# Kernel optimization log

Measured on AMD Instinct MI355X. Metric: run time of the kernel, lower is better.

## Reference

```python
import jax, jax.numpy as jnp
import numpy as np

SHIFT = 1  # fixed shift_direction (module draws +/-1 at random; we pin +1)

def setup_inputs() -> dict:
    key = jax.random.key(0)
    kx, kw = jax.random.split(key)
    x = jax.random.normal(kx, (1024, 256, 7, 7), dtype=jnp.float32)
    W = jax.random.normal(kw, (128, 3, 3, 512), dtype=jnp.float32)
    return {"x": x, "W": W}

def _fwd(x, W):
    B = x.shape[0]
    t = x.reshape(B, 256, 7, 7)
    # unfold((3,1), padding=(1,0)) along H: t[b,c,k,h,w] = x_pad[b,c,h+k-1,w]
    xp = jnp.pad(t, ((0, 0), (0, 0), (1, 1), (0, 0)))
    t = jnp.stack([xp[:, :, k:k + 7, :] for k in range(3)], axis=2)  # (B,256,3,7,7)
    t = t.reshape(B, 2, 128, 3, 7, 7).transpose(0, 2, 3, 4, 1, 5)   # (B,128,3,7,2,7)
    t = t.reshape(B, 128, 3, 14, 7)
    t = jnp.roll(t, SHIFT, axis=3)
    t = t.reshape(B, 128, 3, 7, 2, 7).sum(axis=4)                   # (B,128,3,7,7)
    t = t.transpose(0, 1, 3, 2, 4)                                  # (B,128,7,3,7)
    t = jnp.roll(t, SHIFT, axis=4)
    # second unfold((3,1), padding=(1,0)) along W dim: gather 3 shifted slices
    tp = jnp.pad(t, ((0, 0), (0, 0), (0, 0), (0, 0), (1, 1)))
    t3 = jnp.stack([tp[..., k2:k2 + 7] for k2 in range(3)], axis=-1)  # (B,128,7,3,7,3) = (m,l,n,j,o,k)
    out = jnp.einsum('mlnjok,ljki->mnoi', t3, W)                     # (B,7,7,512)
    return out.transpose(0, 3, 1, 2)                                 # (B,512,7,7)

def reference(x, W):
    return _fwd(x, W)
```

## Files before the change

kernel.cpp:

```cpp
#include <hip/hip_runtime.h>

typedef __attribute__((ext_vector_type(8)))  __bf16 bvec8;
typedef __attribute__((ext_vector_type(4)))  __bf16 bvec4;
typedef __attribute__((ext_vector_type(16))) float  fvec16;
typedef __attribute__((ext_vector_type(8)))  short  svec8;

__global__ __launch_bounds__(256) void pack_w(const float* __restrict__ W,
                                              __bf16* __restrict__ Wp) {
    int u = blockIdx.x * 256 + threadIdx.x;
    if (u >= 73728) return;
    int lane = u & 63;
    int h    = (u >> 6) & 1;
    int it   = (u >> 7) & 15;
    int t    = u >> 11;
    int i  = (it << 5) + (lane & 31);
    int K0 = ((2 * t + h) << 4) + ((lane >> 5) << 3);
    bvec8 o;
#pragma unroll
    for (int e = 0; e < 8; ++e) {
        int K  = K0 + e;
        int jk = K >> 7;
        int l  = K & 127;
        int j  = (jk * 11) >> 5;
        int k  = jk - 3 * j;
        o[e] = (__bf16)W[((l * 9 + j * 3 + k) << 9) + i];
    }
    *(bvec8*)&Wp[(size_t)u * 8] = o;
}

__global__ __launch_bounds__(512, 4) void conv_mfma(
    const float* __restrict__ x, const __bf16* __restrict__ Wp,
    float* __restrict__ out)
{
    __shared__ __align__(16) char smem[45056];
    __bf16* xs = (__bf16*)smem;
    __bf16* ys = (__bf16*)(smem + 25088);

    const int tid  = threadIdx.x;
    const int lane = tid & 63;
    const int l31  = lane & 31;
    const int ls5  = lane >> 5;
    const int wi   = tid >> 6;
    const int b    = blockIdx.x;

    const float* xb  = x + (size_t)b * 12544;
    const char*  WpB = (const char*)Wp;
    const int wbase  = wi * 4096 + lane * 16;

    bvec8 aE[2][2], aO[2][2];
#pragma unroll
    for (int am = 0; am < 2; ++am)
#pragma unroll
        for (int h = 0; h < 2; ++h) {
            aE[am][h] = *(const bvec8*)(WpB + wbase + am * 2048 + h * 1024);
            aO[am][h] = *(const bvec8*)(WpB + 32768 + wbase + am * 2048 + h * 1024);
        }

    for (int it = 0; it < 7; ++it) {
        int e4 = it * 512 + tid;
        if (e4 < 3136) {
            const float4 v = ((const float4*)xb)[e4];
            bvec4 pk = { (__bf16)v.x, (__bf16)v.y, (__bf16)v.z, (__bf16)v.w };
            *(bvec4*)&xs[e4 * 4] = pk;
        }
    }
    __syncthreads();
    for (int it = 0; it < 3; ++it) {
        int up = it * 512 + tid;
        if (up < 1248) {
            int row  = up >> 4;
            int useg = up & 15;
            int l0   = useg * 8;
            bvec8 ov;
            if (row == 77) {
                ov = __builtin_bit_cast(bvec8, (svec8)0);
            } else if (row < 63) {
                int t = row / 7, w = row - t * 7;
                int tb = t + 5; if (tb >= 7) tb -= 7;
                int cB = tb * 7 + w;
                bool mA = (t >= 1) && (t <= 7);
                int cA = mA ? (t - 1) * 7 + w : 0;
#pragma unroll
                for (int d = 0; d < 8; ++d) {
                    float fa = mA ? (float)xs[(l0 + d) * 49 + cA] : 0.f;
                    float fb = (float)xs[(128 + l0 + d) * 49 + cB];
                    ov[d] = (__bf16)(fa + fb);
                }
            } else if (row < 70) {
                int w = row - 63;
#pragma unroll
                for (int d = 0; d < 8; ++d) ov[d] = xs[(l0 + d) * 49 + w];
            } else {
                int w = row - 70;
#pragma unroll
                for (int d = 0; d < 8; ++d) ov[d] = xs[(l0 + d) * 49 + 7 + w];
            }
            *(bvec8*)&ys[(row << 7) + ((useg ^ (row & 15)) << 3)] = ov;
        }
    }

    int nq[2], oo[2];
#pragma unroll
    for (int sn = 0; sn < 2; ++sn) {
        int s = sn * 32 + l31;
        int sc = (s < 49) ? s : 48;
        nq[sn] = sc / 7;
        oo[sn] = sc - nq[sn] * 7;
    }

    fvec16 acc[2][2];
#pragma unroll
    for (int am = 0; am < 2; ++am)
#pragma unroll
        for (int sn = 0; sn < 2; ++sn)
#pragma unroll
            for (int r = 0; r < 16; ++r) acc[am][sn][r] = 0.f;

    __syncthreads();

    {
        const int zz = (wi & 3) + ((wi >> 2) << 1);
        for (int z = 0; z < zz; ++z) __builtin_amdgcn_s_sleep(8);
    }

#define GEO(JK) {                                                             \
        int j_ = ((JK) * 11) >> 5; int k_ = (JK) - 3 * j_;                    \
        _Pragma("unroll")                                                     \
        for (int sn_ = 0; sn_ < 2; ++sn_) {                                   \
            int tw_ = oo[sn_] + k_ + 5; int w_ = tw_ >= 7 ? tw_ - 7 : tw_;    \
            int row_ = (nq[sn_] + j_) * 7 + w_;                               \
            if (nq[sn_] == 1 && j_ == 0) row_ = 63 + w_;                      \
            if (nq[sn_] == 0 && j_ == 2) row_ = 70 + w_;                      \
            if ((k_ == 0 && oo[sn_] == 0) || (k_ == 2 && oo[sn_] == 6))       \
                row_ = 77;                                                    \
            rowE[sn_] = (row_) << 7; rx[sn_] = row_ & 15; } }

#define STEP(P, AW, TNEXT, DOPF) {                                            \
        _Pragma("unroll")                                                     \
        for (int h_ = 0; h_ < 2; ++h_)                                        \
        _Pragma("unroll")                                                     \
        for (int sn_ = 0; sn_ < 2; ++sn_) {                                   \
            int u_ = ((P) * 4 + h_ * 2 + ls5) ^ rx[sn_];                      \
            bvec8 bf_ = *(const bvec8*)&ys[rowE[sn_] + (u_ << 3)];            \
            __builtin_amdgcn_s_setprio(1);                                    \
            _Pragma("unroll")                                                 \
            for (int am_ = 0; am_ < 2; ++am_)                                 \
                acc[am_][sn_] = __builtin_amdgcn_mfma_f32_32x32x16_bf16(      \
                    AW[am_][h_], bf_, acc[am_][sn_], 0, 0, 0);                \
            __builtin_amdgcn_s_setprio(0);                                    \
        }                                                                     \
        if (DOPF) {                                                           \
            const char* gp_ = WpB + ((size_t)(TNEXT) << 15) + wbase;          \
            _Pragma("unroll")                                                 \
            for (int am_ = 0; am_ < 2; ++am_)                                 \
            _Pragma("unroll")                                                 \
            for (int h_ = 0; h_ < 2; ++h_)                                    \
                AW[am_][h_] = *(const bvec8*)(gp_ + am_ * 2048 + h_ * 1024);  \
        } }

    int rowE[2], rx[2];
    for (int jk = 0; jk < 9; ++jk) {
        const int t0 = jk * 4;
        GEO(jk);
        STEP(0, aE, t0 + 2, true)
        STEP(1, aO, t0 + 3, true)
        STEP(2, aE, t0 + 4, (jk < 8))
        STEP(3, aO, t0 + 5, (jk < 8))
    }

#undef GEO
#undef STEP

    const size_t ob = (size_t)b * 25088;
#pragma unroll
    for (int am = 0; am < 2; ++am) {
        const int i0 = wi * 64 + am * 32 + 4 * ls5;
#pragma unroll
        for (int sn = 0; sn < 2; ++sn) {
            if (sn == 1 && l31 >= 17) continue;
            const int s = sn * 32 + l31;
#pragma unroll
            for (int r = 0; r < 16; ++r) {
                int i = i0 + (r & 3) + 8 * (r >> 2);
                out[ob + (size_t)i * 49 + s] = acc[am][sn][r];
            }
        }
    }
}

extern "C" void kernel_launch(void* const* d_in, const int* in_sizes, int n_in,
                              void* d_out, int out_size, void* d_ws, size_t ws_size,
                              hipStream_t stream) {
    const float* x = (const float*)d_in[0];
    const float* W = (const float*)d_in[1];
    float* out = (float*)d_out;
    __bf16* Wp = (__bf16*)d_ws;
    (void)in_sizes; (void)n_in; (void)out_size; (void)ws_size;

    hipLaunchKernelGGL(pack_w, dim3(288), dim3(256), 0, stream, W, Wp);
    hipLaunchKernelGGL(conv_mfma, dim3(1024), dim3(512), 0, stream, x, Wp, out);
}
```

Before: 96.26 us.

## Tile conv over 4 batches x 256 outputs with LDS-staged double-buffered weights

Each block now handles four batch images and half of the 512 output channels instead of one image and all channels. Weight tiles are streamed into LDS with global_load_lds in a double buffer and shared across all waves, so each weight byte is reused across four images. Before, every wave loaded its own weight fragments from global memory for each image. The cost is large dynamic shared memory (about 142 KB), fewer resident blocks, a barrier after every k-step, and the input-prep phase running serially for the four images.

```diff
diff --git a/kernel.cpp b/kernel.cpp
--- a/kernel.cpp
+++ b/kernel.cpp
@@ -4,17 +4,25 @@
 typedef __attribute__((ext_vector_type(4)))  __bf16 bvec4;
 typedef __attribute__((ext_vector_type(16))) float  fvec16;
 typedef __attribute__((ext_vector_type(8)))  short  svec8;
+
+__device__ __forceinline__ void gload16(const void* g, void* l) {
+    __builtin_amdgcn_global_load_lds(
+        (const __attribute__((address_space(1))) void*)g,
+        (__attribute__((address_space(3))) void*)l,
+        16, 0, 0);
+}
 
 __global__ __launch_bounds__(256) void pack_w(const float* __restrict__ W,
                                               __bf16* __restrict__ Wp) {
     int u = blockIdx.x * 256 + threadIdx.x;
     if (u >= 73728) return;
     int lane = u & 63;
-    int h    = (u >> 6) & 1;
-    int it   = (u >> 7) & 15;
-    int t    = u >> 11;
-    int i  = (it << 5) + (lane & 31);
-    int K0 = ((2 * t + h) << 4) + ((lane >> 5) << 3);
+    int iu   = (u >> 6) & 7;
+    int kk   = (u >> 9) & 3;
+    int ib   = (u >> 11) & 1;
+    int t64  = u >> 12;
+    int i  = ib * 256 + iu * 32 + (lane & 31);
+    int K0 = t64 * 64 + kk * 16 + ((lane >> 5) << 3);
     bvec8 o;
 #pragma unroll
     for (int e = 0; e < 8; ++e) {
@@ -28,75 +36,73 @@
     *(bvec8*)&Wp[(size_t)u * 8] = o;
 }
 
-__global__ __launch_bounds__(512, 4) void conv_mfma(
+__global__ __launch_bounds__(512, 2) void conv_mfma(
     const float* __restrict__ x, const __bf16* __restrict__ Wp,
     float* __restrict__ out)
 {
-    __shared__ __align__(16) char smem[45056];
-    __bf16* xs = (__bf16*)smem;
-    __bf16* ys = (__bf16*)(smem + 25088);
+    extern __shared__ __align__(16) char smem[];
+    __bf16* ys   = (__bf16*)smem;
+    char*  wbufB = smem + 79872;
+    __bf16* xs   = (__bf16*)wbufB;
 
     const int tid  = threadIdx.x;
     const int lane = tid & 63;
     const int l31  = lane & 31;
     const int ls5  = lane >> 5;
-    const int wi   = tid >> 6;
-    const int b    = blockIdx.x;
-
-    const float* xb  = x + (size_t)b * 12544;
+    const int wid  = tid >> 6;
+    const int wq   = wid & 3;
+    const int wm   = wid >> 2;
+    const int bm   = blockIdx.x;
+    const int ib   = blockIdx.y;
+    const int b0   = bm * 4;
+
+    const float* xb  = x + (size_t)b0 * 12544;
     const char*  WpB = (const char*)Wp;
-    const int wbase  = wi * 4096 + lane * 16;
-
-    bvec8 aE[2][2], aO[2][2];
-#pragma unroll
-    for (int am = 0; am < 2; ++am)
-#pragma unroll
-        for (int h = 0; h < 2; ++h) {
-            aE[am][h] = *(const bvec8*)(WpB + wbase + am * 2048 + h * 1024);
-            aO[am][h] = *(const bvec8*)(WpB + 32768 + wbase + am * 2048 + h * 1024);
-        }
-
-    for (int it = 0; it < 7; ++it) {
-        int e4 = it * 512 + tid;
-        if (e4 < 3136) {
-            const float4 v = ((const float4*)xb)[e4];
-            bvec4 pk = { (__bf16)v.x, (__bf16)v.y, (__bf16)v.z, (__bf16)v.w };
-            *(bvec4*)&xs[e4 * 4] = pk;
-        }
-    }
-    __syncthreads();
-    for (int it = 0; it < 3; ++it) {
-        int up = it * 512 + tid;
-        if (up < 1248) {
-            int row  = up >> 4;
-            int useg = up & 15;
-            int l0   = useg * 8;
-            bvec8 ov;
-            if (row == 77) {
-                ov = __builtin_bit_cast(bvec8, (svec8)0);
-            } else if (row < 63) {
-                int t = row / 7, w = row - t * 7;
-                int tb = t + 5; if (tb >= 7) tb -= 7;
-                int cB = tb * 7 + w;
-                bool mA = (t >= 1) && (t <= 7);
-                int cA = mA ? (t - 1) * 7 + w : 0;
-#pragma unroll
-                for (int d = 0; d < 8; ++d) {
-                    float fa = mA ? (float)xs[(l0 + d) * 49 + cA] : 0.f;
-                    float fb = (float)xs[(128 + l0 + d) * 49 + cB];
-                    ov[d] = (__bf16)(fa + fb);
+
+    for (int bb = 0; bb < 4; ++bb) {
+        for (int it = 0; it < 7; ++it) {
+            int e4 = it * 512 + tid;
+            if (e4 < 3136) {
+                const float4 v = ((const float4*)(xb + bb * 12544))[e4];
+                bvec4 pk = { (__bf16)v.x, (__bf16)v.y, (__bf16)v.z, (__bf16)v.w };
+                *(bvec4*)&xs[e4 * 4] = pk;
+            }
+        }
+        __syncthreads();
+        for (int it = 0; it < 3; ++it) {
+            int up = it * 512 + tid;
+            if (up < 1248) {
+                int row  = up >> 4;
+                int useg = up & 15;
+                int l0   = useg * 8;
+                bvec8 ov;
+                if (row == 77) {
+                    ov = __builtin_bit_cast(bvec8, (svec8)0);
+                } else if (row < 63) {
+                    int t = row / 7, w = row - t * 7;
+                    int tb = t + 5; if (tb >= 7) tb -= 7;
+                    int cB = tb * 7 + w;
+                    bool mA = (t >= 1) && (t <= 7);
+                    int cA = mA ? (t - 1) * 7 + w : 0;
+#pragma unroll
+                    for (int d = 0; d < 8; ++d) {
+                        float fa = mA ? (float)xs[(l0 + d) * 49 + cA] : 0.f;
+                        float fb = (float)xs[(128 + l0 + d) * 49 + cB];
+                        ov[d] = (__bf16)(fa + fb);
+                    }
+                } else if (row < 70) {
+                    int w = row - 63;
+#pragma unroll
+                    for (int d = 0; d < 8; ++d) ov[d] = xs[(l0 + d) * 49 + w];
+                } else {
+                    int w = row - 70;
+#pragma unroll
+                    for (int d = 0; d < 8; ++d) ov[d] = xs[(l0 + d) * 49 + 7 + w];
                 }
-            } else if (row < 70) {
-                int w = row - 63;
-#pragma unroll
-                for (int d = 0; d < 8; ++d) ov[d] = xs[(l0 + d) * 49 + w];
-            } else {
-                int w = row - 70;
-#pragma unroll
-                for (int d = 0; d < 8; ++d) ov[d] = xs[(l0 + d) * 49 + 7 + w];
-            }
-            *(bvec8*)&ys[(row << 7) + ((useg ^ (row & 15)) << 3)] = ov;
-        }
+                *(bvec8*)&ys[((bb * 78 + row) << 7) + ((useg ^ (row & 15)) << 3)] = ov;
+            }
+        }
+        __syncthreads();
     }
 
     int nq[2], oo[2];
@@ -107,82 +113,96 @@
         nq[sn] = sc / 7;
         oo[sn] = sc - nq[sn] * 7;
     }
-
-    fvec16 acc[2][2];
-#pragma unroll
-    for (int am = 0; am < 2; ++am)
-#pragma unroll
-        for (int sn = 0; sn < 2; ++sn)
-#pragma unroll
-            for (int r = 0; r < 16; ++r) acc[am][sn][r] = 0.f;
-
-    __syncthreads();
-
-    {
-        const int zz = (wi & 3) + ((wi >> 2) << 1);
-        for (int z = 0; z < zz; ++z) __builtin_amdgcn_s_sleep(8);
-    }
-
-#define GEO(JK) {                                                             \
-        int j_ = ((JK) * 11) >> 5; int k_ = (JK) - 3 * j_;                    \
+    const int bb2[2] = { (2 * wm) * 9984, (2 * wm + 1) * 9984 };
+
+    fvec16 acc[4][2];
+#pragma unroll
+    for (int mt = 0; mt < 4; ++mt)
+#pragma unroll
+        for (int nt = 0; nt < 2; ++nt)
+#pragma unroll
+            for (int r = 0; r < 16; ++r) acc[mt][nt][r] = 0.f;
+
+#define STAGE(T, SLOT) {                                                      \
+        const char* g_ = WpB + (((size_t)(T) * 2 + ib) << 15) + tid * 16;     \
+        char* d_ = wbufB + (SLOT) * 32768 + tid * 16;                         \
         _Pragma("unroll")                                                     \
-        for (int sn_ = 0; sn_ < 2; ++sn_) {                                   \
-            int tw_ = oo[sn_] + k_ + 5; int w_ = tw_ >= 7 ? tw_ - 7 : tw_;    \
-            int row_ = (nq[sn_] + j_) * 7 + w_;                               \
-            if (nq[sn_] == 1 && j_ == 0) row_ = 63 + w_;                      \
-            if (nq[sn_] == 0 && j_ == 2) row_ = 70 + w_;                      \
-            if ((k_ == 0 && oo[sn_] == 0) || (k_ == 2 && oo[sn_] == 6))       \
-                row_ = 77;                                                    \
-            rowE[sn_] = (row_) << 7; rx[sn_] = row_ & 15; } }
-
-#define STEP(P, AW, TNEXT, DOPF) {                                            \
-        _Pragma("unroll")                                                     \
-        for (int h_ = 0; h_ < 2; ++h_)                                        \
-        _Pragma("unroll")                                                     \
-        for (int sn_ = 0; sn_ < 2; ++sn_) {                                   \
-            int u_ = ((P) * 4 + h_ * 2 + ls5) ^ rx[sn_];                      \
-            bvec8 bf_ = *(const bvec8*)&ys[rowE[sn_] + (u_ << 3)];            \
-            __builtin_amdgcn_s_setprio(1);                                    \
-            _Pragma("unroll")                                                 \
-            for (int am_ = 0; am_ < 2; ++am_)                                 \
-                acc[am_][sn_] = __builtin_amdgcn_mfma_f32_32x32x16_bf16(      \
-                    AW[am_][h_], bf_, acc[am_][sn_], 0, 0, 0);                \
-            __builtin_amdgcn_s_setprio(0);                                    \
-        }                                                                     \
-        if (DOPF) {                                                           \
-            const char* gp_ = WpB + ((size_t)(TNEXT) << 15) + wbase;          \
-            _Pragma("unroll")                                                 \
-            for (int am_ = 0; am_ < 2; ++am_)                                 \
-            _Pragma("unroll")                                                 \
-            for (int h_ = 0; h_ < 2; ++h_)                                    \
-                AW[am_][h_] = *(const bvec8*)(gp_ + am_ * 2048 + h_ * 1024);  \
-        } }
+        for (int r_ = 0; r_ < 4; ++r_)                                        \
+            gload16(g_ + r_ * 8192, d_ + r_ * 8192);                          \
+    }
+
+#define BARRIER() { asm volatile("" ::: "memory");                            \
+        __builtin_amdgcn_s_barrier();                                         \
+        asm volatile("" ::: "memory"); }
+
+    STAGE(0, 0)
+    STAGE(1, 1)
 
     int rowE[2], rx[2];
     for (int jk = 0; jk < 9; ++jk) {
-        const int t0 = jk * 4;
-        GEO(jk);
-        STEP(0, aE, t0 + 2, true)
-        STEP(1, aO, t0 + 3, true)
-        STEP(2, aE, t0 + 4, (jk < 8))
-        STEP(3, aO, t0 + 5, (jk < 8))
-    }
-
-#undef GEO
-#undef STEP
-
-    const size_t ob = (size_t)b * 25088;
-#pragma unroll
-    for (int am = 0; am < 2; ++am) {
-        const int i0 = wi * 64 + am * 32 + 4 * ls5;
-#pragma unroll
-        for (int sn = 0; sn < 2; ++sn) {
-            if (sn == 1 && l31 >= 17) continue;
-            const int s = sn * 32 + l31;
+        {
+            int j_ = (jk * 11) >> 5; int k_ = jk - 3 * j_;
+#pragma unroll
+            for (int sn = 0; sn < 2; ++sn) {
+                int tw = oo[sn] + k_ + 5; int w = tw >= 7 ? tw - 7 : tw;
+                int row = (nq[sn] + j_) * 7 + w;
+                if (nq[sn] == 1 && j_ == 0) row = 63 + w;
+                if (nq[sn] == 0 && j_ == 2) row = 70 + w;
+                if ((k_ == 0 && oo[sn] == 0) || (k_ == 2 && oo[sn] == 6)) row = 77;
+                rowE[sn] = row << 7; rx[sn] = row & 15;
+            }
+        }
+#pragma unroll
+        for (int half = 0; half < 2; ++half) {
+            const int t   = jk * 2 + half;
+            const int cur = t & 1;
+            if (t == 17) { asm volatile("s_waitcnt vmcnt(0)" ::: "memory"); }
+            else        { asm volatile("s_waitcnt vmcnt(4)" ::: "memory"); }
+            BARRIER()
+            const char* ws = wbufB + cur * 32768;
+#pragma unroll
+            for (int p = 0; p < 4; ++p) {
+                bvec8 wa[2], bf[4];
+#pragma unroll
+                for (int nt = 0; nt < 2; ++nt)
+                    wa[nt] = *(const bvec8*)(ws + ((p * 8 + wq * 2 + nt) << 10)
+                                             + lane * 16);
+#pragma unroll
+                for (int mt = 0; mt < 4; ++mt) {
+                    const int sn = mt & 1;
+                    const int u  = (half * 8 + p * 2 + ls5) ^ rx[sn];
+                    bf[mt] = *(const bvec8*)&ys[bb2[mt >> 1] + rowE[sn] + (u << 3)];
+                }
+                __builtin_amdgcn_s_setprio(1);
+#pragma unroll
+                for (int mt = 0; mt < 4; ++mt)
+#pragma unroll
+                    for (int nt = 0; nt < 2; ++nt)
+                        acc[mt][nt] = __builtin_amdgcn_mfma_f32_32x32x16_bf16(
+                            wa[nt], bf[mt], acc[mt][nt], 0, 0, 0);
+                __builtin_amdgcn_s_setprio(0);
+                BARRIER()
+            }
+            if (t + 2 < 18) STAGE(t + 2, cur)
+        }
+    }
+
+#undef STAGE
+#undef BARRIER
+
+#pragma unroll
+    for (int mt = 0; mt < 4; ++mt) {
+        const int sn = mt & 1;
+        if (sn == 1 && l31 >= 17) continue;
+        const int s = sn * 32 + l31;
+        const size_t ob = (size_t)(b0 + 2 * wm + (mt >> 1)) * 25088;
+#pragma unroll
+        for (int nt = 0; nt < 2; ++nt) {
+            const int i0 = ib * 256 + wq * 64 + nt * 32 + 4 * ls5;
 #pragma unroll
             for (int r = 0; r < 16; ++r) {
                 int i = i0 + (r & 3) + 8 * (r >> 2);
-                out[ob + (size_t)i * 49 + s] = acc[am][sn][r];
+                out[ob + (size_t)i * 49 + s] = acc[mt][nt][r];
             }
         }
     }
@@ -197,6 +217,9 @@
     __bf16* Wp = (__bf16*)d_ws;
     (void)in_sizes; (void)n_in; (void)out_size; (void)ws_size;
 
+    hipFuncSetAttribute(reinterpret_cast<const void*>(conv_mfma),
+                        hipFuncAttributeMaxDynamicSharedMemorySize, 145408);
+
     hipLaunchKernelGGL(pack_w, dim3(288), dim3(256), 0, stream, W, Wp);
-    hipLaunchKernelGGL(conv_mfma, dim3(1024), dim3(512), 0, stream, x, Wp, out);
-}
+    hipLaunchKernelGGL(conv_mfma, dim3(256, 2), dim3(512), 145408, stream, x, Wp, out);
+}
```

Result: slower. 112.1 us (+16.5%).

## Split activation prep into separate kernel and tile GEMM over flattened batch-spatial rows

Applied to the files above, without the earlier changes.

Moves the per-sample input transform (bf16 conversion, roll/sum/unfold gather) into a new build_ys kernel that writes a swizzled bf16 buffer to workspace. The conv kernel now tiles the flattened (batch*49) spatial dimension in 128-row chunks across up to 4 samples, with 2 output-channel halves per grid column. Tiles are loaded into LDS via global_load_lds, which removes the wasted padded columns (49 of 64) of the old per-sample tiling. In exchange it adds an extra kernel launch and a global round trip for the intermediate, uses more LDS (lower occupancy), and drops the staggered wave sleep.

```diff
diff --git a/kernel.cpp b/kernel.cpp
--- a/kernel.cpp
+++ b/kernel.cpp
@@ -4,6 +4,13 @@
 typedef __attribute__((ext_vector_type(4)))  __bf16 bvec4;
 typedef __attribute__((ext_vector_type(16))) float  fvec16;
 typedef __attribute__((ext_vector_type(8)))  short  svec8;
+
+__device__ __forceinline__ void gload16(const void* g, void* l) {
+    __builtin_amdgcn_global_load_lds(
+        (const __attribute__((address_space(1))) void*)g,
+        (__attribute__((address_space(3))) void*)l,
+        16, 0, 0);
+}
 
 __global__ __launch_bounds__(256) void pack_w(const float* __restrict__ W,
                                               __bf16* __restrict__ Wp) {
@@ -28,36 +35,14 @@
     *(bvec8*)&Wp[(size_t)u * 8] = o;
 }
 
-__global__ __launch_bounds__(512, 4) void conv_mfma(
-    const float* __restrict__ x, const __bf16* __restrict__ Wp,
-    float* __restrict__ out)
-{
-    __shared__ __align__(16) char smem[45056];
-    __bf16* xs = (__bf16*)smem;
-    __bf16* ys = (__bf16*)(smem + 25088);
-
-    const int tid  = threadIdx.x;
-    const int lane = tid & 63;
-    const int l31  = lane & 31;
-    const int ls5  = lane >> 5;
-    const int wi   = tid >> 6;
-    const int b    = blockIdx.x;
-
-    const float* xb  = x + (size_t)b * 12544;
-    const char*  WpB = (const char*)Wp;
-    const int wbase  = wi * 4096 + lane * 16;
-
-    bvec8 aE[2][2], aO[2][2];
-#pragma unroll
-    for (int am = 0; am < 2; ++am)
-#pragma unroll
-        for (int h = 0; h < 2; ++h) {
-            aE[am][h] = *(const bvec8*)(WpB + wbase + am * 2048 + h * 1024);
-            aO[am][h] = *(const bvec8*)(WpB + 32768 + wbase + am * 2048 + h * 1024);
-        }
-
-    for (int it = 0; it < 7; ++it) {
-        int e4 = it * 512 + tid;
+__global__ __launch_bounds__(256) void build_ys(const float* __restrict__ x,
+                                                __bf16* __restrict__ ysG) {
+    __shared__ __bf16 xs[12544];
+    const int tid = threadIdx.x;
+    const int b   = blockIdx.x;
+    const float* xb = x + (size_t)b * 12544;
+    for (int it = 0; it < 13; ++it) {
+        int e4 = it * 256 + tid;
         if (e4 < 3136) {
             const float4 v = ((const float4*)xb)[e4];
             bvec4 pk = { (__bf16)v.x, (__bf16)v.y, (__bf16)v.z, (__bf16)v.w };
@@ -65,8 +50,9 @@
         }
     }
     __syncthreads();
-    for (int it = 0; it < 3; ++it) {
-        int up = it * 512 + tid;
+    char* yb = (char*)ysG + (size_t)b * 19968;
+    for (int it = 0; it < 5; ++it) {
+        int up = it * 256 + tid;
         if (up < 1248) {
             int row  = up >> 4;
             int useg = up & 15;
@@ -95,67 +81,112 @@
 #pragma unroll
                 for (int d = 0; d < 8; ++d) ov[d] = xs[(l0 + d) * 49 + 7 + w];
             }
-            *(bvec8*)&ys[(row << 7) + ((useg ^ (row & 15)) << 3)] = ov;
-        }
-    }
-
-    int nq[2], oo[2];
-#pragma unroll
-    for (int sn = 0; sn < 2; ++sn) {
-        int s = sn * 32 + l31;
-        int sc = (s < 49) ? s : 48;
-        nq[sn] = sc / 7;
-        oo[sn] = sc - nq[sn] * 7;
+            *(bvec8*)(yb + (row << 8) + ((useg ^ (row & 15)) << 4)) = ov;
+        }
+    }
+}
+
+__global__ __launch_bounds__(512, 4) void conv_mfma(
+    const __bf16* __restrict__ ysG, const __bf16* __restrict__ Wp,
+    float* __restrict__ out)
+{
+    extern __shared__ __align__(16) char smem[];
+    __bf16* ys = (__bf16*)smem;
+
+    const int tid  = threadIdx.x;
+    const int lane = tid & 63;
+    const int l31  = lane & 31;
+    const int ls5  = lane >> 5;
+    const int wid  = tid >> 6;
+    const int wn   = wid & 3;
+    const int wm   = wid >> 2;
+    const int ib   = blockIdx.y;
+    const int g0   = blockIdx.x * 128;
+    const int bb0  = g0 / 49;
+
+    const char* WpB = (const char*)Wp;
+    const int wbase = (ib * 8 + wn * 2) * 2048 + lane * 16;
+
+    bvec8 aE[2][2], aO[2][2];
+#pragma unroll
+    for (int nt = 0; nt < 2; ++nt)
+#pragma unroll
+        for (int h = 0; h < 2; ++h) {
+            aE[nt][h] = *(const bvec8*)(WpB + wbase + nt * 2048 + h * 1024);
+            aO[nt][h] = *(const bvec8*)(WpB + 32768 + wbase + nt * 2048 + h * 1024);
+        }
+
+    {
+        const char* ysGB = (const char*)ysG;
+#pragma unroll
+        for (int r = 0; r < 10; ++r) {
+            int v = r * 512 + tid;
+            if (v < 4992) {
+                int sl  = v / 1248;
+                int off = v - sl * 1248;
+                int bsl = bb0 + sl; if (bsl > 1023) bsl = 1023;
+                gload16(ysGB + (size_t)bsl * 19968 + off * 16,
+                        smem + v * 16);
+            }
+        }
+    }
+
+    int ysb[2], nq[2], oo[2], bOut[2], sOut[2];
+#pragma unroll
+    for (int mt = 0; mt < 2; ++mt) {
+        int g  = g0 + (wm * 2 + mt) * 32 + l31;
+        int bb = g / 49;
+        int s  = g - bb * 49;
+        ysb[mt]  = (bb - bb0) * 9984;
+        nq[mt]   = s / 7;
+        oo[mt]   = s - nq[mt] * 7;
+        bOut[mt] = bb;
+        sOut[mt] = s;
     }
 
     fvec16 acc[2][2];
 #pragma unroll
-    for (int am = 0; am < 2; ++am)
-#pragma unroll
-        for (int sn = 0; sn < 2; ++sn)
-#pragma unroll
-            for (int r = 0; r < 16; ++r) acc[am][sn][r] = 0.f;
+    for (int mt = 0; mt < 2; ++mt)
+#pragma unroll
+        for (int nt = 0; nt < 2; ++nt)
+#pragma unroll
+            for (int r = 0; r < 16; ++r) acc[mt][nt][r] = 0.f;
 
     __syncthreads();
-
-    {
-        const int zz = (wi & 3) + ((wi >> 2) << 1);
-        for (int z = 0; z < zz; ++z) __builtin_amdgcn_s_sleep(8);
-    }
 
 #define GEO(JK) {                                                             \
         int j_ = ((JK) * 11) >> 5; int k_ = (JK) - 3 * j_;                    \
         _Pragma("unroll")                                                     \
-        for (int sn_ = 0; sn_ < 2; ++sn_) {                                   \
-            int tw_ = oo[sn_] + k_ + 5; int w_ = tw_ >= 7 ? tw_ - 7 : tw_;    \
-            int row_ = (nq[sn_] + j_) * 7 + w_;                               \
-            if (nq[sn_] == 1 && j_ == 0) row_ = 63 + w_;                      \
-            if (nq[sn_] == 0 && j_ == 2) row_ = 70 + w_;                      \
-            if ((k_ == 0 && oo[sn_] == 0) || (k_ == 2 && oo[sn_] == 6))       \
+        for (int mt_ = 0; mt_ < 2; ++mt_) {                                   \
+            int tw_ = oo[mt_] + k_ + 5; int w_ = tw_ >= 7 ? tw_ - 7 : tw_;    \
+            int row_ = (nq[mt_] + j_) * 7 + w_;                               \
+            if (nq[mt_] == 1 && j_ == 0) row_ = 63 + w_;                      \
+            if (nq[mt_] == 0 && j_ == 2) row_ = 70 + w_;                      \
+            if ((k_ == 0 && oo[mt_] == 0) || (k_ == 2 && oo[mt_] == 6))       \
                 row_ = 77;                                                    \
-            rowE[sn_] = (row_) << 7; rx[sn_] = row_ & 15; } }
+            rowE[mt_] = ysb[mt_] + (row_ << 7); rx[mt_] = row_ & 15; } }
 
 #define STEP(P, AW, TNEXT, DOPF) {                                            \
         _Pragma("unroll")                                                     \
         for (int h_ = 0; h_ < 2; ++h_)                                        \
         _Pragma("unroll")                                                     \
-        for (int sn_ = 0; sn_ < 2; ++sn_) {                                   \
-            int u_ = ((P) * 4 + h_ * 2 + ls5) ^ rx[sn_];                      \
-            bvec8 bf_ = *(const bvec8*)&ys[rowE[sn_] + (u_ << 3)];            \
+        for (int mt_ = 0; mt_ < 2; ++mt_) {                                   \
+            int u_ = ((P) * 4 + h_ * 2 + ls5) ^ rx[mt_];                      \
+            bvec8 bf_ = *(const bvec8*)&ys[rowE[mt_] + (u_ << 3)];            \
             __builtin_amdgcn_s_setprio(1);                                    \
             _Pragma("unroll")                                                 \
-            for (int am_ = 0; am_ < 2; ++am_)                                 \
-                acc[am_][sn_] = __builtin_amdgcn_mfma_f32_32x32x16_bf16(      \
-                    AW[am_][h_], bf_, acc[am_][sn_], 0, 0, 0);                \
+            for (int nt_ = 0; nt_ < 2; ++nt_)                                 \
+                acc[mt_][nt_] = __builtin_amdgcn_mfma_f32_32x32x16_bf16(      \
+                    AW[nt_][h_], bf_, acc[mt_][nt_], 0, 0, 0);                \
             __builtin_amdgcn_s_setprio(0);                                    \
         }                                                                     \
         if (DOPF) {                                                           \
             const char* gp_ = WpB + ((size_t)(TNEXT) << 15) + wbase;          \
             _Pragma("unroll")                                                 \
-            for (int am_ = 0; am_ < 2; ++am_)                                 \
+            for (int nt_ = 0; nt_ < 2; ++nt_)                                 \
             _Pragma("unroll")                                                 \
             for (int h_ = 0; h_ < 2; ++h_)                                    \
-                AW[am_][h_] = *(const bvec8*)(gp_ + am_ * 2048 + h_ * 1024);  \
+                AW[nt_][h_] = *(const bvec8*)(gp_ + nt_ * 2048 + h_ * 1024);  \
         } }
 
     int rowE[2], rx[2];
@@ -171,18 +202,16 @@
 #undef GEO
 #undef STEP
 
-    const size_t ob = (size_t)b * 25088;
-#pragma unroll
-    for (int am = 0; am < 2; ++am) {
-        const int i0 = wi * 64 + am * 32 + 4 * ls5;
-#pragma unroll
-        for (int sn = 0; sn < 2; ++sn) {
-            if (sn == 1 && l31 >= 17) continue;
-            const int s = sn * 32 + l31;
+#pragma unroll
+    for (int mt = 0; mt < 2; ++mt) {
+        const size_t ob = (size_t)bOut[mt] * 25088 + sOut[mt];
+#pragma unroll
+        for (int nt = 0; nt < 2; ++nt) {
+            const int i0 = ib * 256 + wn * 64 + nt * 32 + 4 * ls5;
 #pragma unroll
             for (int r = 0; r < 16; ++r) {
                 int i = i0 + (r & 3) + 8 * (r >> 2);
-                out[ob + (size_t)i * 49 + s] = acc[am][sn][r];
+                out[ob + (size_t)i * 49] = acc[mt][nt][r];
             }
         }
     }
@@ -194,9 +223,15 @@
     const float* x = (const float*)d_in[0];
     const float* W = (const float*)d_in[1];
     float* out = (float*)d_out;
-    __bf16* Wp = (__bf16*)d_ws;
+    __bf16* Wp  = (__bf16*)d_ws;
+    __bf16* ysG = (__bf16*)((char*)d_ws + 1179648);
     (void)in_sizes; (void)n_in; (void)out_size; (void)ws_size;
 
+    hipFuncSetAttribute(reinterpret_cast<const void*>(conv_mfma),
+                        hipFuncAttributeMaxDynamicSharedMemorySize, 79872);
+
     hipLaunchKernelGGL(pack_w, dim3(288), dim3(256), 0, stream, W, Wp);
-    hipLaunchKernelGGL(conv_mfma, dim3(1024), dim3(512), 0, stream, x, Wp, out);
-}
+    hipLaunchKernelGGL(build_ys, dim3(1024), dim3(256), 0, stream, x, ysG);
+    hipLaunchKernelGGL(conv_mfma, dim3(392, 2), dim3(512), 79872, stream,
+                       ysG, Wp, out);
+}
```

Result: slower. 106.9 us (+11.0%).
